# Optimization experiments

Hardware: AMD Instinct MI355X
Metric: run time of the kernel (lower is better)

The kernel has to match this reference:

```python
import jax, jax.numpy as jnp
import numpy as np

EPS = 1e-12
B, DIN, T, DH = 32, 512, 4096, 500


def setup_inputs() -> dict:
    key = jax.random.key(0)
    k1, k2, k3 = jax.random.split(key, 3)
    x = jax.random.normal(k1, (B, DIN, T), dtype=jnp.float32)
    weight1 = jax.random.normal(k2, (DH, DIN), dtype=jnp.float32) * (1.0 / np.sqrt(DIN))
    weight2 = jax.random.normal(k3, (1, DH), dtype=jnp.float32) * (1.0 / np.sqrt(DH))
    return {"x": x, "weight1": weight1, "weight2": weight2, "dim": 2}


def reference(x, weight1, weight2, dim):
    # x: (B, din, T)
    h = jnp.swapaxes(x, 1, 2)                      # (B, T, din)
    a = jax.nn.relu(jnp.einsum('btd,hd->bth', h, weight1))  # (B, T, dh)
    scores = jnp.einsum('bth,oh->bto', a, weight2)           # (B, T, 1)
    attn = jax.nn.softmax(scores, axis=1)                    # softmax over time
    mean = jnp.einsum('bdt,bto->bdo', x, attn)               # (B, din, 1)
    variance = jnp.mean((x - mean) ** 2, axis=dim)           # (B, din) unweighted
    mean_s = jnp.squeeze(mean, axis=dim)                     # (B, din)
    mask = (variance <= EPS).astype(variance.dtype)
    variance = (1.0 - mask) * variance + mask * EPS
    stddev = jnp.sqrt(variance)
    return jnp.concatenate((mean_s, stddev), axis=-1)        # (B, 2*din)
```

## Files before the change

### kernel.cpp

```cpp
#include <hip/hip_runtime.h>
#include <hip/hip_bf16.h>

#define NB 32
#define DIN 512
#define TT 4096
#define DH 500
#define DHP 512
#define EPSV 1e-12f
#define BM 64
#define LDA 520
#define NTILES (TT / BM)

typedef short short8 __attribute__((ext_vector_type(8)));
typedef float f32x16 __attribute__((ext_vector_type(16)));
typedef float f32x4 __attribute__((ext_vector_type(4)));

__device__ inline unsigned short f2bf(float f) {
    unsigned int u = __builtin_bit_cast(unsigned int, f);
    unsigned int r = (u + 0x7fffu + ((u >> 16) & 1u)) >> 16;
    return (unsigned short)r;
}
__device__ inline float bf2f(unsigned short h) {
    unsigned int u = ((unsigned int)h) << 16;
    return __builtin_bit_cast(float, u);
}

__global__ void prep_kernel(const float* __restrict__ w1, const float* __restrict__ w2,
                            unsigned short* __restrict__ w1b, float* __restrict__ w2f) {
    int idx = blockIdx.x * blockDim.x + threadIdx.x;
    if (idx < DHP * DIN) {
        const int j    = idx & 7;
        const int lane = (idx >> 3) & 63;
        const int ks   = (idx >> 9) & 31;
        const int hb   = idx >> 14;
        const int h = hb * 32 + (lane & 31);
        const int d = ks * 16 + (lane >> 5) * 8 + j;
        float v = (h < DH) ? w1[h * DIN + d] : 0.f;
        w1b[idx] = f2bf(v);
        if (idx < DHP) w2f[idx] = (idx < DH) ? w2[idx] : 0.f;
    }
}

__launch_bounds__(512, 4)
__global__ void scores_fused(const float* __restrict__ x,
                             const unsigned short* __restrict__ w1b,
                             const float* __restrict__ w2f,
                             float* __restrict__ pm, float* __restrict__ pz,
                             float* __restrict__ pswx, float* __restrict__ psx,
                             float* __restrict__ psx2) {
    __shared__ unsigned short A_lds[BM][LDA];
    __shared__ float score_p[8][BM];
    __shared__ float w_lds[BM];

    const int tid = threadIdx.x;
    const int b = blockIdx.x >> 6;
    const int t0 = (blockIdx.x & 63) * BM;

    {
        const int ts = tid & 63;
        const int dg = tid >> 6;
        const float* xb = x + (size_t)b * DIN * TT + t0 + ts;
        #pragma unroll
        for (int oct = 0; oct < 8; ++oct) {
            const int d0 = dg * 64 + oct * 8;
            short8 pk;
            #pragma unroll
            for (int j = 0; j < 8; ++j)
                pk[j] = (short)f2bf(xb[(size_t)(d0 + j) * TT]);
            *reinterpret_cast<short8*>(&A_lds[ts][d0]) = pk;
        }
    }
    __syncthreads();

    const int w = tid >> 6;
    const int lane = tid & 63;
    const int lane31 = lane & 31;
    const int khalf = lane >> 5;
    const int hrow0 = w * 64;

    f32x16 acc00, acc01, acc10, acc11;
    #pragma unroll
    for (int g = 0; g < 16; ++g) { acc00[g] = 0.f; acc01[g] = 0.f; acc10[g] = 0.f; acc11[g] = 0.f; }

    const unsigned short* base0 = w1b + (size_t)w * 32768 + (size_t)lane * 8;
    const unsigned short* base1 = base0 + 16384;
    const unsigned short* Bp0 = &A_lds[lane31][khalf * 8];
    const unsigned short* Bp1 = &A_lds[32 + lane31][khalf * 8];

    #pragma unroll 4
    for (int ks = 0; ks < 32; ++ks) {
        short8 a0 = *reinterpret_cast<const short8*>(base0 + ks * 512);
        short8 a1 = *reinterpret_cast<const short8*>(base1 + ks * 512);
        short8 b0 = *reinterpret_cast<const short8*>(Bp0 + ks * 16);
        short8 b1 = *reinterpret_cast<const short8*>(Bp1 + ks * 16);
        acc00 = __builtin_amdgcn_mfma_f32_32x32x16_bf16(a0, b0, acc00, 0, 0, 0);
        acc01 = __builtin_amdgcn_mfma_f32_32x32x16_bf16(a0, b1, acc01, 0, 0, 0);
        acc10 = __builtin_amdgcn_mfma_f32_32x32x16_bf16(a1, b0, acc10, 0, 0, 0);
        acc11 = __builtin_amdgcn_mfma_f32_32x32x16_bf16(a1, b1, acc11, 0, 0, 0);
    }

    float s0 = 0.f, s1 = 0.f;
    #pragma unroll
    for (int g = 0; g < 16; ++g) {
        const int rp = (g & 3) + 8 * (g >> 2) + 4 * khalf;
        const float w20 = w2f[hrow0 + rp];
        const float w21 = w2f[hrow0 + 32 + rp];
        s0 += fmaxf(acc00[g], 0.f) * w20 + fmaxf(acc10[g], 0.f) * w21;
        s1 += fmaxf(acc01[g], 0.f) * w20 + fmaxf(acc11[g], 0.f) * w21;
    }
    s0 += __shfl_xor(s0, 32, 64);
    s1 += __shfl_xor(s1, 32, 64);
    if (khalf == 0) {
        score_p[w][lane31] = s0;
        score_p[w][32 + lane31] = s1;
    }
    __syncthreads();

    if (tid < BM) {
        float s = 0.f;
        #pragma unroll
        for (int ww = 0; ww < 8; ++ww) s += score_p[ww][tid];
        float m = s;
        #pragma unroll
        for (int k = 1; k <= 32; k <<= 1) m = fmaxf(m, __shfl_xor(m, k, 64));
        float e = __expf(s - m);
        float Z = e;
        #pragma unroll
        for (int k = 1; k <= 32; k <<= 1) Z += __shfl_xor(Z, k, 64);
        w_lds[tid] = e;
        if (tid == 0) { pm[blockIdx.x] = m; pz[blockIdx.x] = Z; }
    }
    __syncthreads();

    {
        const int d = tid;
        float sx = 0.f, sx2 = 0.f, swx = 0.f;
        #pragma unroll 8
        for (int t = 0; t < BM; ++t) {
            const float xv = bf2f(A_lds[t][d]);
            const float wv = w_lds[t];
            sx += xv; sx2 += xv * xv; swx += wv * xv;
        }
        const size_t o = (size_t)blockIdx.x * DHP + d;
        psx[o] = sx; psx2[o] = sx2; pswx[o] = swx;
    }
}

__global__ void combine_kernel(const float* __restrict__ pm, const float* __restrict__ pz,
                               const float* __restrict__ pswx, const float* __restrict__ psx,
                               const float* __restrict__ psx2, float* __restrict__ out) {
    __shared__ float sm[NTILES], sz[NTILES];
    const int b = blockIdx.x;
    const int tid = threadIdx.x;
    if (tid < NTILES) { sm[tid] = pm[b * NTILES + tid]; sz[tid] = pz[b * NTILES + tid]; }
    __syncthreads();

    float mg = -1e30f;
    #pragma unroll 8
    for (int i = 0; i < NTILES; ++i) mg = fmaxf(mg, sm[i]);
    float denom = 0.f;
    #pragma unroll 8
    for (int i = 0; i < NTILES; ++i) denom += sz[i] * __expf(sm[i] - mg);

    float num = 0.f, sx = 0.f, sx2 = 0.f;
    #pragma unroll 4
    for (int i = 0; i < NTILES; ++i) {
        const size_t o = ((size_t)(b * NTILES + i)) * DHP + tid;
        const float f = __expf(sm[i] - mg);
        num += f * pswx[o];
        sx  += psx[o];
        sx2 += psx2[o];
    }
    const float mean = num / denom;
    const float ex  = sx  * (1.f / TT);
    const float ex2 = sx2 * (1.f / TT);
    float var = ex2 - 2.f * mean * ex + mean * mean;
    if (var <= EPSV) var = EPSV;
    out[(size_t)b * 1024 + tid] = mean;
    out[(size_t)b * 1024 + 512 + tid] = sqrtf(var);
}

extern "C" void kernel_launch(void* const* d_in, const int* in_sizes, int n_in,
                              void* d_out, int out_size, void* d_ws, size_t ws_size,
                              hipStream_t stream) {
    const float* x  = (const float*)d_in[0];
    const float* w1 = (const float*)d_in[1];
    const float* w2 = (const float*)d_in[2];
    float* out = (float*)d_out;

    char* ws = (char*)d_ws;
    unsigned short* w1b = (unsigned short*)ws;
    float* w2f  = (float*)(ws + 524288);
    float* pm   = (float*)(ws + 526336);
    float* pz   = (float*)(ws + 534528);
    float* pswx = (float*)(ws + 542720);
    float* psx  = pswx + (size_t)NB * NTILES * DHP;
    float* psx2 = psx  + (size_t)NB * NTILES * DHP;

    prep_kernel<<<(DHP * DIN + 255) / 256, 256, 0, stream>>>(w1, w2, w1b, w2f);
    scores_fused<<<NB * NTILES, 512, 0, stream>>>(x, w1b, w2f, pm, pz, pswx, psx, psx2);
    combine_kernel<<<NB, 512, 0, stream>>>(pm, pz, pswx, psx, psx2, out);
}
```

Before: 124.2 us.

## Make scores kernel persistent over 8 time tiles with double-buffered x prefetch

```diff
diff --git a/kernel.cpp b/kernel.cpp
--- a/kernel.cpp
+++ b/kernel.cpp
@@ -10,10 +10,10 @@
 #define BM 64
 #define LDA 520
 #define NTILES (TT / BM)
+#define TPB 8
 
 typedef short short8 __attribute__((ext_vector_type(8)));
 typedef float f32x16 __attribute__((ext_vector_type(16)));
-typedef float f32x4 __attribute__((ext_vector_type(4)));
 
 __device__ inline unsigned short f2bf(float f) {
     unsigned int u = __builtin_bit_cast(unsigned int, f);
@@ -41,36 +41,23 @@
     }
 }
 
-__launch_bounds__(512, 4)
+__launch_bounds__(512, 2)
 __global__ void scores_fused(const float* __restrict__ x,
                              const unsigned short* __restrict__ w1b,
                              const float* __restrict__ w2f,
                              float* __restrict__ pm, float* __restrict__ pz,
                              float* __restrict__ pswx, float* __restrict__ psx,
                              float* __restrict__ psx2) {
-    __shared__ unsigned short A_lds[BM][LDA];
+    __shared__ unsigned short A_lds[2][BM][LDA];
     __shared__ float score_p[8][BM];
-    __shared__ float w_lds[BM];
+    __shared__ float w_lds[2][BM];
 
     const int tid = threadIdx.x;
-    const int b = blockIdx.x >> 6;
-    const int t0 = (blockIdx.x & 63) * BM;
-
-    {
-        const int ts = tid & 63;
-        const int dg = tid >> 6;
-        const float* xb = x + (size_t)b * DIN * TT + t0 + ts;
-        #pragma unroll
-        for (int oct = 0; oct < 8; ++oct) {
-            const int d0 = dg * 64 + oct * 8;
-            short8 pk;
-            #pragma unroll
-            for (int j = 0; j < 8; ++j)
-                pk[j] = (short)f2bf(xb[(size_t)(d0 + j) * TT]);
-            *reinterpret_cast<short8*>(&A_lds[ts][d0]) = pk;
-        }
-    }
-    __syncthreads();
+    const int b  = blockIdx.x >> 3;
+    const int tg = blockIdx.x & 7;
+
+    const int ts = tid & 63;
+    const int dg = tid >> 6;
 
     const int w = tid >> 6;
     const int lane = tid & 63;
@@ -78,71 +65,120 @@
     const int khalf = lane >> 5;
     const int hrow0 = w * 64;
 
-    f32x16 acc00, acc01, acc10, acc11;
-    #pragma unroll
-    for (int g = 0; g < 16; ++g) { acc00[g] = 0.f; acc01[g] = 0.f; acc10[g] = 0.f; acc11[g] = 0.f; }
-
-    const unsigned short* base0 = w1b + (size_t)w * 32768 + (size_t)lane * 8;
-    const unsigned short* base1 = base0 + 16384;
-    const unsigned short* Bp0 = &A_lds[lane31][khalf * 8];
-    const unsigned short* Bp1 = &A_lds[32 + lane31][khalf * 8];
-
-    #pragma unroll 4
-    for (int ks = 0; ks < 32; ++ks) {
-        short8 a0 = *reinterpret_cast<const short8*>(base0 + ks * 512);
-        short8 a1 = *reinterpret_cast<const short8*>(base1 + ks * 512);
-        short8 b0 = *reinterpret_cast<const short8*>(Bp0 + ks * 16);
-        short8 b1 = *reinterpret_cast<const short8*>(Bp1 + ks * 16);
-        acc00 = __builtin_amdgcn_mfma_f32_32x32x16_bf16(a0, b0, acc00, 0, 0, 0);
-        acc01 = __builtin_amdgcn_mfma_f32_32x32x16_bf16(a0, b1, acc01, 0, 0, 0);
-        acc10 = __builtin_amdgcn_mfma_f32_32x32x16_bf16(a1, b0, acc10, 0, 0, 0);
-        acc11 = __builtin_amdgcn_mfma_f32_32x32x16_bf16(a1, b1, acc11, 0, 0, 0);
-    }
-
-    float s0 = 0.f, s1 = 0.f;
+    float w20v[16], w21v[16];
     #pragma unroll
     for (int g = 0; g < 16; ++g) {
         const int rp = (g & 3) + 8 * (g >> 2) + 4 * khalf;
-        const float w20 = w2f[hrow0 + rp];
-        const float w21 = w2f[hrow0 + 32 + rp];
-        s0 += fmaxf(acc00[g], 0.f) * w20 + fmaxf(acc10[g], 0.f) * w21;
-        s1 += fmaxf(acc01[g], 0.f) * w20 + fmaxf(acc11[g], 0.f) * w21;
-    }
-    s0 += __shfl_xor(s0, 32, 64);
-    s1 += __shfl_xor(s1, 32, 64);
-    if (khalf == 0) {
-        score_p[w][lane31] = s0;
-        score_p[w][32 + lane31] = s1;
+        w20v[g] = w2f[hrow0 + rp];
+        w21v[g] = w2f[hrow0 + 32 + rp];
+    }
+
+    const float* xbase = x + (size_t)b * DIN * TT;
+    const unsigned short* base0 = w1b + (size_t)w * 32768 + (size_t)lane * 8;
+    const unsigned short* base1 = base0 + 16384;
+
+    {
+        const float* xb = xbase + (size_t)(tg * TPB) * BM + ts;
+        #pragma unroll
+        for (int oct = 0; oct < 8; ++oct) {
+            short8 pk;
+            #pragma unroll
+            for (int j = 0; j < 8; ++j)
+                pk[j] = (short)f2bf(xb[(size_t)(dg * 64 + oct * 8 + j) * TT]);
+            *reinterpret_cast<short8*>(&A_lds[0][ts][dg * 64 + oct * 8]) = pk;
+        }
     }
     __syncthreads();
 
-    if (tid < BM) {
-        float s = 0.f;
+    for (int i = 0; i < TPB; ++i) {
+        const int buf = i & 1;
+        const bool more = (i + 1 < TPB);
+
+        float xr[64];
+        if (more) {
+            const float* xb = xbase + (size_t)(tg * TPB + i + 1) * BM + ts;
+            #pragma unroll
+            for (int oct = 0; oct < 8; ++oct)
+                #pragma unroll
+                for (int j = 0; j < 8; ++j)
+                    xr[oct * 8 + j] = xb[(size_t)(dg * 64 + oct * 8 + j) * TT];
+        }
+
+        f32x16 acc00, acc01, acc10, acc11;
         #pragma unroll
-        for (int ww = 0; ww < 8; ++ww) s += score_p[ww][tid];
-        float m = s;
+        for (int g = 0; g < 16; ++g) { acc00[g] = 0.f; acc01[g] = 0.f; acc10[g] = 0.f; acc11[g] = 0.f; }
+
+        const unsigned short* Bp0 = &A_lds[buf][lane31][khalf * 8];
+        const unsigned short* Bp1 = &A_lds[buf][32 + lane31][khalf * 8];
+
+        #pragma unroll 4
+        for (int ks = 0; ks < 32; ++ks) {
+            short8 a0 = *reinterpret_cast<const short8*>(base0 + ks * 512);
+            short8 a1 = *reinterpret_cast<const short8*>(base1 + ks * 512);
+            short8 b0 = *reinterpret_cast<const short8*>(Bp0 + ks * 16);
+            short8 b1 = *reinterpret_cast<const short8*>(Bp1 + ks * 16);
+            acc00 = __builtin_amdgcn_mfma_f32_32x32x16_bf16(a0, b0, acc00, 0, 0, 0);
+            acc01 = __builtin_amdgcn_mfma_f32_32x32x16_bf16(a0, b1, acc01, 0, 0, 0);
+            acc10 = __builtin_amdgcn_mfma_f32_32x32x16_bf16(a1, b0, acc10, 0, 0, 0);
+            acc11 = __builtin_amdgcn_mfma_f32_32x32x16_bf16(a1, b1, acc11, 0, 0, 0);
+        }
+
+        float s0 = 0.f, s1 = 0.f;
         #pragma unroll
-        for (int k = 1; k <= 32; k <<= 1) m = fmaxf(m, __shfl_xor(m, k, 64));
-        float e = __expf(s - m);
-        float Z = e;
-        #pragma unroll
-        for (int k = 1; k <= 32; k <<= 1) Z += __shfl_xor(Z, k, 64);
-        w_lds[tid] = e;
-        if (tid == 0) { pm[blockIdx.x] = m; pz[blockIdx.x] = Z; }
-    }
-    __syncthreads();
-
-    {
-        const int d = tid;
-        float sx = 0.f, sx2 = 0.f, swx = 0.f;
-        #pragma unroll 8
-        for (int t = 0; t < BM; ++t) {
-            const float xv = bf2f(A_lds[t][d]);
-            const float wv = w_lds[t];
-            sx += xv; sx2 += xv * xv; swx += wv * xv;
-        }
-        const size_t o = (size_t)blockIdx.x * DHP + d;
-        psx[o] = sx; psx2[o] = sx2; pswx[o] = swx;
+        for (int g = 0; g < 16; ++g) {
+            s0 += fmaxf(acc00[g], 0.f) * w20v[g] + fmaxf(acc10[g], 0.f) * w21v[g];
+            s1 += fmaxf(acc01[g], 0.f) * w20v[g] + fmaxf(acc11[g], 0.f) * w21v[g];
+        }
+        s0 += __shfl_xor(s0, 32, 64);
+        s1 += __shfl_xor(s1, 32, 64);
+        if (khalf == 0) {
+            score_p[w][lane31] = s0;
+            score_p[w][32 + lane31] = s1;
+        }
+        __syncthreads();
+
+        if (tid < BM) {
+            float s = 0.f;
+            #pragma unroll
+            for (int ww = 0; ww < 8; ++ww) s += score_p[ww][tid];
+            float m = s;
+            #pragma unroll
+            for (int k = 1; k <= 32; k <<= 1) m = fmaxf(m, __shfl_xor(m, k, 64));
+            float e = __expf(s - m);
+            float Z = e;
+            #pragma unroll
+            for (int k = 1; k <= 32; k <<= 1) Z += __shfl_xor(Z, k, 64);
+            w_lds[buf][tid] = e;
+            if (tid == 0) {
+                const size_t gt = (size_t)blockIdx.x * TPB + i;
+                pm[gt] = m; pz[gt] = Z;
+            }
+        }
+        __syncthreads();
+
+        {
+            const int d = tid;
+            float sx = 0.f, sx2 = 0.f, swx = 0.f;
+            #pragma unroll 8
+            for (int t = 0; t < BM; ++t) {
+                const float xv = bf2f(A_lds[buf][t][d]);
+                const float wv = w_lds[buf][t];
+                sx += xv; sx2 += xv * xv; swx += wv * xv;
+            }
+            const size_t o = ((size_t)blockIdx.x * TPB + i) * DHP + d;
+            psx[o] = sx; psx2[o] = sx2; pswx[o] = swx;
+        }
+
+        if (more) {
+            #pragma unroll
+            for (int oct = 0; oct < 8; ++oct) {
+                short8 pk;
+                #pragma unroll
+                for (int j = 0; j < 8; ++j) pk[j] = (short)f2bf(xr[oct * 8 + j]);
+                *reinterpret_cast<short8*>(&A_lds[buf ^ 1][ts][dg * 64 + oct * 8]) = pk;
+            }
+        }
+        __syncthreads();
     }
 }
 
@@ -198,6 +234,6 @@
     float* psx2 = psx  + (size_t)NB * NTILES * DHP;
 
     prep_kernel<<<(DHP * DIN + 255) / 256, 256, 0, stream>>>(w1, w2, w1b, w2f);
-    scores_fused<<<NB * NTILES, 512, 0, stream>>>(x, w1b, w2f, pm, pz, pswx, psx, psx2);
+    scores_fused<<<NB * TPB, 512, 0, stream>>>(x, w1b, w2f, pm, pz, pswx, psx, psx2);
     combine_kernel<<<NB, 512, 0, stream>>>(pm, pz, pswx, psx, psx2, out);
 }
```

New measurement: 150.8 us. 1.21x slower.
